# Optimization experiments

Hardware: AMD Instinct MI355X
Metric: run time of the kernel (lower is better)

Reference implementation:

```python
import jax, jax.numpy as jnp
import numpy as np

B, N, C, H = 1, 2048, 1024, 16


def setup_inputs() -> dict:
    key = jax.random.key(0)
    ks = jax.random.split(key, 8)
    scale = 1.0 / np.sqrt(C)
    d = {"x": jax.random.normal(ks[0], (B, N, C), dtype=jnp.float32)}
    for i, name in enumerate(["q1", "q2", "k1", "k2", "v", "out"]):
        d[f"W_{name}"] = jax.random.normal(ks[1 + i], (C, C), dtype=jnp.float32) * scale
        d[f"b_{name}"] = jnp.zeros((C,), dtype=jnp.float32)
    d["ln_g"] = jnp.ones((C,), dtype=jnp.float32)
    d["ln_b"] = jnp.zeros((C,), dtype=jnp.float32)
    return d


def reference(x, W_q1, b_q1, W_q2, b_q2, W_k1, b_k1, W_k2, b_k2,
              W_v, b_v, W_out, b_out, ln_g, ln_b):
    Bx, Nx, Cx = x.shape
    hd = Cx // H  # head_dim

    def proj(W, b):
        # ResidualMLP with num_layers=-1 and in_dim==out_dim: x + Linear(x)
        return x + x @ W + b

    def split_heads(z):
        return z.reshape(Bx, Nx, H, hd).transpose(0, 2, 1, 3)  # b h n d

    # kernel='identity', norm_q=norm_k=False -> raw projections
    q1 = split_heads(proj(W_q1, b_q1))
    q2 = split_heads(proj(W_q2, b_q2))
    k1 = split_heads(proj(W_k1, b_k1))
    k2 = split_heads(proj(W_k2, b_k2))
    v = split_heads(proj(W_v, b_v))

    # triple attention: elementwise product of the two Gram matrices, then
    # row-normalized (flash-style softmax; kernel also returns lse which the
    # module discards: `_, out = self.attn(...)`)
    s = jnp.einsum('bhnd,bhmd->bhnm', q1, k1) * jnp.einsum('bhnd,bhmd->bhnm', q2, k2)
    p = jax.nn.softmax(s, axis=-1)
    o = jnp.einsum('bhnm,bhmd->bhnd', p, v)

    o = o.transpose(0, 2, 1, 3).reshape(Bx, Nx, Cx)  # b n (h d)

    # LayerNorm (eps=1e-5, torch default)
    mu = o.mean(axis=-1, keepdims=True)
    var = ((o - mu) ** 2).mean(axis=-1, keepdims=True)
    o = (o - mu) / jnp.sqrt(var + 1e-5) * ln_g + ln_b

    return o @ W_out + b_out
```

## Files before the change

### kernel.cpp

```cpp
#include <hip/hip_runtime.h>
#include <hip/hip_bf16.h>
#include <stdint.h>


#define N_SEQ 2048
#define CDIM  1024
#define NHEAD 16
#define HDIM  64

typedef __attribute__((ext_vector_type(8))) short bfrag;
typedef __attribute__((ext_vector_type(4))) float f4;
typedef __attribute__((ext_vector_type(16))) float f16v;
typedef unsigned short u16;

#define MFMA16(a, b, c) __builtin_amdgcn_mfma_f32_16x16x32_bf16((a), (b), (c), 0, 0, 0)
#define MFMA32(a, b, c) __builtin_amdgcn_mfma_f32_32x32x16_bf16((a), (b), (c), 0, 0, 0)

__device__ __forceinline__ float bf2f(u16 u) {
  union { unsigned int i; float f; } c; c.i = ((unsigned int)u) << 16; return c.f;
}
__device__ __forceinline__ u16 f2bf(float f) {
  union { float f; unsigned int i; } c; c.f = f;
  unsigned int i = c.i;
  return (u16)((i + 0x7FFFu + ((i >> 16) & 1u)) >> 16);
}
__device__ __forceinline__ unsigned int pk2(float lo, float hi) {
  __hip_bfloat162 b = __float22bfloat162_rn(make_float2(lo, hi));
  unsigned int u;
  __builtin_memcpy(&u, &b, 4);
  return u;
}

__device__ __forceinline__ void gld16(const void* g, void* lds) {
  __builtin_amdgcn_global_load_lds(
      (const __attribute__((address_space(1))) void*)g,
      (__attribute__((address_space(3))) void*)lds, 16, 0, 0);
}

__global__ __launch_bounds__(256) void k_split_x(
    const float* __restrict__ x, u16* __restrict__ xh, u16* __restrict__ xl) {
  int i = (blockIdx.x * 256 + threadIdx.x) * 4;
  float4 v = *(const float4*)(x + i);
  float vv[4] = {v.x, v.y, v.z, v.w};
  ushort4 h, l;
  u16 hh[4], ll[4];
#pragma unroll
  for (int j = 0; j < 4; j++) {
    hh[j] = f2bf(vv[j]);
    ll[j] = f2bf(vv[j] - bf2f(hh[j]));
  }
  h.x = hh[0]; h.y = hh[1]; h.z = hh[2]; h.w = hh[3];
  l.x = ll[0]; l.y = ll[1]; l.z = ll[2]; l.w = ll[3];
  *(ushort4*)(xh + i) = h;
  *(ushort4*)(xl + i) = l;
}

__global__ __launch_bounds__(256) void k_wsplit(
    const float* __restrict__ W0, const float* __restrict__ W1,
    const float* __restrict__ W2, const float* __restrict__ W3,
    const float* __restrict__ W4, const float* __restrict__ W5,
    u16* __restrict__ wth, u16* __restrict__ wtl) {
  __shared__ float tile[64][65];
  int wz = blockIdx.z;
  const float* W = wz == 0 ? W0 : wz == 1 ? W1 : wz == 2 ? W2 : wz == 3 ? W3 : wz == 4 ? W4 : W5;
  int kb = blockIdx.x * 64, nb = blockIdx.y * 64;
  int t = threadIdx.x;
  int r0 = t >> 4, c0 = (t & 15) * 4;
#pragma unroll
  for (int i = 0; i < 4; i++) {
    int r = r0 + i * 16;
    float4 v = *(const float4*)(W + (size_t)(kb + r) * CDIM + nb + c0);
    tile[r][c0 + 0] = v.x; tile[r][c0 + 1] = v.y; tile[r][c0 + 2] = v.z; tile[r][c0 + 3] = v.w;
  }
  __syncthreads();
#pragma unroll
  for (int i = 0; i < 4; i++) {
    int wn = (t >> 4) + i * 16;
    int wk = (t & 15) * 4;
    ushort4 h, l;
    u16 hh[4], ll[4];
#pragma unroll
    for (int j = 0; j < 4; j++) {
      float v = tile[wk + j][wn];
      hh[j] = f2bf(v);
      ll[j] = f2bf(v - bf2f(hh[j]));
    }
    h.x = hh[0]; h.y = hh[1]; h.z = hh[2]; h.w = hh[3];
    l.x = ll[0]; l.y = ll[1]; l.z = ll[2]; l.w = ll[3];
    size_t off = ((size_t)wz * CDIM + nb + wn) * CDIM + kb + wk;
    *(ushort4*)(wth + off) = h;
    if (wz < 4) *(ushort4*)(wtl + off) = l;
  }
}

__global__ __launch_bounds__(256, 2) void k_proj(
    const u16* __restrict__ xh, const u16* __restrict__ xl,
    const u16* __restrict__ wth, const u16* __restrict__ wtl,
    const float* __restrict__ x,
    const float* __restrict__ b0, const float* __restrict__ b1,
    const float* __restrict__ b2, const float* __restrict__ b3,
    const float* __restrict__ b4,
    u16* __restrict__ qh, u16* __restrict__ ql, u16* __restrict__ vT) {
  __shared__ u16 sA[128 * 64];
  __shared__ u16 sB[128 * 64];
  int t = threadIdx.x;
  int w = blockIdx.x >> 3;
  int n0 = (blockIdx.x & 7) * 128;
  int m0 = blockIdx.y * 128;
  int lane = t & 63, wid = t >> 6;
  int wm = (wid >> 1) * 64, wn = (wid & 1) * 64;
  int lr = lane & 15, lg = lane >> 4;

  f4 acc[4][4];
#pragma unroll
  for (int i = 0; i < 4; i++)
#pragma unroll
    for (int j = 0; j < 4; j++) acc[i][j] = (f4)0.0f;

  const int nphase = (w < 4) ? 3 : 1;
  const u16* wb = wth + (size_t)w * CDIM * CDIM;
  const u16* wl = wtl + (size_t)w * CDIM * CDIM;

  int srow = t >> 3;
  int scol = (t & 7) * 8;
  int soff = srow * 64 + scol;

  for (int p = 0; p < nphase; p++) {
    const u16* A = (p == 2) ? xl : xh;
    const u16* B = (p == 1) ? wl : wb;
    for (int kt = 0; kt < CDIM; kt += 64) {
#pragma unroll
      for (int c = 0; c < 4; c++) {
        gld16(A + (size_t)(m0 + srow + c * 32) * CDIM + kt + scol, (u16*)sA + soff + c * 2048);
        gld16(B + (size_t)(n0 + srow + c * 32) * CDIM + kt + scol, (u16*)sB + soff + c * 2048);
      }
      __syncthreads();
#pragma unroll
      for (int kk = 0; kk < 2; kk++) {
        bfrag af[4], bv[4];
#pragma unroll
        for (int mi = 0; mi < 4; mi++)
          af[mi] = *(const bfrag*)(sA + (wm + mi * 16 + lr) * 64 + kk * 32 + lg * 8);
#pragma unroll
        for (int ni = 0; ni < 4; ni++)
          bv[ni] = *(const bfrag*)(sB + (wn + ni * 16 + lr) * 64 + kk * 32 + lg * 8);
#pragma unroll
        for (int mi = 0; mi < 4; mi++)
#pragma unroll
          for (int ni = 0; ni < 4; ni++)
            acc[mi][ni] = MFMA16(af[mi], bv[ni], acc[mi][ni]);
      }
      __syncthreads();
    }
  }

  const float* bias = w == 0 ? b0 : w == 1 ? b1 : w == 2 ? b2 : w == 3 ? b3 : b4;
#pragma unroll
  for (int mi = 0; mi < 4; mi++) {
#pragma unroll
    for (int ni = 0; ni < 4; ni++) {
      int col = n0 + wn + ni * 16 + lr;
      int rowb = m0 + wm + mi * 16 + lg * 4;
      float vv[4];
#pragma unroll
      for (int r = 0; r < 4; r++)
        vv[r] = acc[mi][ni][r] + x[(size_t)(rowb + r) * CDIM + col] + bias[col];
      if (w < 4) {
#pragma unroll
        for (int r = 0; r < 4; r++) {
          u16 h = f2bf(vv[r]);
          u16 l = f2bf(vv[r] - bf2f(h));
          qh[((size_t)w * N_SEQ + rowb + r) * CDIM + col] = h;
          ql[((size_t)w * N_SEQ + rowb + r) * CDIM + col] = l;
        }
      } else {
        ushort4 pv;
        pv.x = f2bf(vv[0]); pv.y = f2bf(vv[1]); pv.z = f2bf(vv[2]); pv.w = f2bf(vv[3]);
        *(ushort4*)(vT + (size_t)col * N_SEQ + rowb) = pv;
      }
    }
  }
}

__global__ __launch_bounds__(256, 2) void k_attn(
    const u16* __restrict__ qkh, const u16* __restrict__ qkl,
    const u16* __restrict__ vT, u16* __restrict__ O0, u16* __restrict__ O1,
    float2* __restrict__ ml) {
  __shared__ u16 sbuf[2][32 * 512];
  int bid = blockIdx.x;
  int khalf = bid >> 8;
  int inner = bid & 255;
  int vb = (inner & 7) * 32 + (inner >> 3);
  int h = vb >> 4;
  int qb = (vb & 15) * 128;
  int t = threadIdx.x, lane = t & 63, wv = t >> 6;
  int l31 = lane & 31, hi5 = lane >> 5;
  const size_t NC = (size_t)N_SEQ * CDIM;
  const int hoff = h * HDIM;
  const int k0 = khalf * (N_SEQ / 2);
  u16* Op = khalf ? O1 : O0;

  int qrow = qb + wv * 32 + l31;
  bfrag q1h[4], q1l[4], q2h[4], q2l[4];
#pragma unroll
  for (int ks = 0; ks < 4; ks++) {
    size_t off = (size_t)qrow * CDIM + hoff + ks * 16 + hi5 * 8;
    q1h[ks] = *(const bfrag*)(qkh + off);
    q1l[ks] = *(const bfrag*)(qkl + off);
    q2h[ks] = *(const bfrag*)(qkh + NC + off);
    q2l[ks] = *(const bfrag*)(qkl + NC + off);
  }

  const u16* kb = ((wv & 1) ? qkl : qkh) + (size_t)(2 + (wv >> 1)) * NC;

  float mrun = -1e30f, lrun = 0.f;
  f16v accO0 = (f16v)0.0f, accO1 = (f16v)0.0f;

#define STAGE(bi, kt)                                                          \
  {                                                                            \
    _Pragma("unroll") for (int i = 0; i < 8; i++) {                            \
      int kh_ = i >> 2, ksp_ = i & 3;                                          \
      gld16(kb + (size_t)((kt) + kh_ * 32 + l31) * CDIM + hoff + ksp_ * 16 +   \
                hi5 * 8,                                                       \
            sbuf[bi] + ((wv * 8 + i) << 9));                                   \
    }                                                                          \
  }

  STAGE(0, k0);
  asm volatile("s_waitcnt vmcnt(0)" ::: "memory");
  __builtin_amdgcn_s_barrier();

#pragma unroll 1
  for (int it = 0; it < N_SEQ / 2 / 64; it++) {
    int kt = k0 + it * 64;
    if (it + 1 < N_SEQ / 2 / 64) STAGE((it + 1) & 1, kt + 64);

    bfrag vld[2][4];
#pragma unroll
    for (int kh = 0; kh < 2; kh++) {
      const u16* vb0 = vT + (size_t)(hoff + l31) * N_SEQ + kt + kh * 32 + hi5 * 8;
      const u16* vb1 = vT + (size_t)(hoff + 32 + l31) * N_SEQ + kt + kh * 32 + hi5 * 8;
      vld[kh][0] = *(const bfrag*)(vb0);
      vld[kh][1] = *(const bfrag*)(vb0 + 16);
      vld[kh][2] = *(const bfrag*)(vb1);
      vld[kh][3] = *(const bfrag*)(vb1 + 16);
    }

    const u16* sb = sbuf[it & 1];
    f16v s1[2], s2[2];
#pragma unroll
    for (int kh = 0; kh < 2; kh++) { s1[kh] = (f16v)0.0f; s2[kh] = (f16v)0.0f; }
#pragma unroll
    for (int kh = 0; kh < 2; kh++) {
#pragma unroll
      for (int ks = 0; ks < 4; ks++) {
        const u16* cb = sb + ((kh * 4 + ks) << 9) + lane * 8;
        bfrag k1h = *(const bfrag*)(cb);
        bfrag k1l = *(const bfrag*)(cb + (8 << 9));
        bfrag k2h = *(const bfrag*)(cb + (16 << 9));
        bfrag k2l = *(const bfrag*)(cb + (24 << 9));
        s1[kh] = MFMA32(k1h, q1h[ks], s1[kh]);
        s1[kh] = MFMA32(k1h, q1l[ks], s1[kh]);
        s1[kh] = MFMA32(k1l, q1h[ks], s1[kh]);
        s2[kh] = MFMA32(k2h, q2h[ks], s2[kh]);
        s2[kh] = MFMA32(k2h, q2l[ks], s2[kh]);
        s2[kh] = MFMA32(k2l, q2h[ks], s2[kh]);
      }
    }
    f16v p0 = s1[0] * s2[0];
    f16v p1 = s1[1] * s2[1];

    float pm = fmaxf(p0[0], p1[0]);
#pragma unroll
    for (int j = 1; j < 16; j++) pm = fmaxf(pm, fmaxf(p0[j], p1[j]));
    pm = fmaxf(pm, __shfl_xor(pm, 32, 64));
    if (__any(pm > mrun + 8.0f)) {
      float mnew = fmaxf(mrun, pm);
      float sc = __expf(mrun - mnew);
      lrun *= sc;
#pragma unroll
      for (int j = 0; j < 16; j++) { accO0[j] *= sc; accO1[j] *= sc; }
      mrun = mnew;
    }
    float rs = 0.f;
#pragma unroll
    for (int j = 0; j < 16; j++) { p0[j] = __expf(p0[j] - mrun); rs += p0[j]; }
#pragma unroll
    for (int j = 0; j < 16; j++) { p1[j] = __expf(p1[j] - mrun); rs += p1[j]; }
    rs += __shfl_xor(rs, 32, 64);
    lrun += rs;

    unsigned dw[16];
#pragma unroll
    for (int j = 0; j < 8; j++) dw[j] = pk2(p0[2 * j], p0[2 * j + 1]);
#pragma unroll
    for (int j = 0; j < 8; j++) dw[8 + j] = pk2(p1[2 * j], p1[2 * j + 1]);

#pragma unroll
    for (int kh = 0; kh < 2; kh++) {
      unsigned j0 = dw[kh * 8 + 0], j1 = dw[kh * 8 + 1], j2 = dw[kh * 8 + 2],
               j3 = dw[kh * 8 + 3], j4 = dw[kh * 8 + 4], j5 = dw[kh * 8 + 5],
               j6 = dw[kh * 8 + 6], j7 = dw[kh * 8 + 7];
      unsigned pj0 = __shfl_xor(j0, 32, 64), pj1 = __shfl_xor(j1, 32, 64);
      unsigned pj2 = __shfl_xor(j2, 32, 64), pj3 = __shfl_xor(j3, 32, 64);
      unsigned pj4 = __shfl_xor(j4, 32, 64), pj5 = __shfl_xor(j5, 32, 64);
      unsigned pj6 = __shfl_xor(j6, 32, 64), pj7 = __shfl_xor(j7, 32, 64);
      union { unsigned u[4]; bfrag b; } f0, f1;
      f0.u[0] = hi5 ? pj2 : j0;
      f0.u[1] = hi5 ? pj3 : j1;
      f0.u[2] = hi5 ? j2 : pj0;
      f0.u[3] = hi5 ? j3 : pj1;
      f1.u[0] = hi5 ? pj6 : j4;
      f1.u[1] = hi5 ? pj7 : j5;
      f1.u[2] = hi5 ? j6 : pj4;
      f1.u[3] = hi5 ? j7 : pj5;
      accO0 = MFMA32(vld[kh][0], f0.b, accO0);
      accO0 = MFMA32(vld[kh][1], f1.b, accO0);
      accO1 = MFMA32(vld[kh][2], f0.b, accO1);
      accO1 = MFMA32(vld[kh][3], f1.b, accO1);
    }

    asm volatile("s_waitcnt vmcnt(0)" ::: "memory");
    __builtin_amdgcn_s_barrier();
  }
#undef STAGE

#pragma unroll
  for (int q4 = 0; q4 < 4; q4++) {
    ushort4 s0, s1v;
    s0.x = f2bf(accO0[q4 * 4 + 0]); s0.y = f2bf(accO0[q4 * 4 + 1]);
    s0.z = f2bf(accO0[q4 * 4 + 2]); s0.w = f2bf(accO0[q4 * 4 + 3]);
    s1v.x = f2bf(accO1[q4 * 4 + 0]); s1v.y = f2bf(accO1[q4 * 4 + 1]);
    s1v.z = f2bf(accO1[q4 * 4 + 2]); s1v.w = f2bf(accO1[q4 * 4 + 3]);
    *(ushort4*)(Op + (size_t)qrow * CDIM + hoff + q4 * 8 + hi5 * 4) = s0;
    *(ushort4*)(Op + (size_t)qrow * CDIM + hoff + 32 + q4 * 8 + hi5 * 4) = s1v;
  }
  if (!hi5) ml[(size_t)(khalf * NHEAD + h) * N_SEQ + qrow] = make_float2(mrun, lrun);
}

__global__ __launch_bounds__(256) void k_cln(
    const u16* __restrict__ O0, const u16* __restrict__ O1,
    const float2* __restrict__ ml, const float* __restrict__ g,
    const float* __restrict__ b, u16* __restrict__ oln) {
  __shared__ float rsm[4], rs2m[4];
  int row = blockIdx.x, t = threadIdx.x;
  int h = t >> 4;
  float2 a = ml[(size_t)h * N_SEQ + row];
  float2 bb = ml[(size_t)(NHEAD + h) * N_SEQ + row];
  float M = fmaxf(a.x, bb.x);
  float w0 = __expf(a.x - M), w1 = __expf(bb.x - M);
  float invL = 1.0f / (w0 * a.y + w1 * bb.y);
  ushort4 u0 = *(const ushort4*)(O0 + (size_t)row * CDIM + t * 4);
  ushort4 u1 = *(const ushort4*)(O1 + (size_t)row * CDIM + t * 4);
  float vals[4];
  vals[0] = (w0 * bf2f(u0.x) + w1 * bf2f(u1.x)) * invL;
  vals[1] = (w0 * bf2f(u0.y) + w1 * bf2f(u1.y)) * invL;
  vals[2] = (w0 * bf2f(u0.z) + w1 * bf2f(u1.z)) * invL;
  vals[3] = (w0 * bf2f(u0.w) + w1 * bf2f(u1.w)) * invL;
  float s = vals[0] + vals[1] + vals[2] + vals[3];
  float s2 = vals[0] * vals[0] + vals[1] * vals[1] + vals[2] * vals[2] + vals[3] * vals[3];
#pragma unroll
  for (int d = 1; d < 64; d <<= 1) {
    s += __shfl_xor(s, d, 64);
    s2 += __shfl_xor(s2, d, 64);
  }
  int wv = t >> 6;
  if ((t & 63) == 0) { rsm[wv] = s; rs2m[wv] = s2; }
  __syncthreads();
  s = rsm[0] + rsm[1] + rsm[2] + rsm[3];
  s2 = rs2m[0] + rs2m[1] + rs2m[2] + rs2m[3];
  float mu = s * (1.0f / CDIM);
  float var = s2 * (1.0f / CDIM) - mu * mu;
  float inv = rsqrtf(var + 1e-5f);
  ushort4 r4;
  u16 rr[4];
#pragma unroll
  for (int j = 0; j < 4; j++) {
    int col = t * 4 + j;
    rr[j] = f2bf((vals[j] - mu) * inv * g[col] + b[col]);
  }
  r4.x = rr[0]; r4.y = rr[1]; r4.z = rr[2]; r4.w = rr[3];
  *(ushort4*)(oln + (size_t)row * CDIM + t * 4) = r4;
}

__global__ __launch_bounds__(256, 2) void k_ogemm(
    const u16* __restrict__ A, const u16* __restrict__ Bw,
    const float* __restrict__ bias, float* __restrict__ out) {
  __shared__ u16 sA[128 * 64];
  __shared__ u16 sB[128 * 64];
  int t = threadIdx.x;
  int n0 = blockIdx.x * 128, m0 = blockIdx.y * 128;
  int lane = t & 63, wid = t >> 6;
  int wm = (wid >> 1) * 64, wn = (wid & 1) * 64;
  int lr = lane & 15, lg = lane >> 4;
  f4 acc[4][4];
#pragma unroll
  for (int i = 0; i < 4; i++)
#pragma unroll
    for (int j = 0; j < 4; j++) acc[i][j] = (f4)0.0f;
  int srow = t >> 3, scol = (t & 7) * 8, soff = srow * 64 + scol;
  for (int kt = 0; kt < CDIM; kt += 64) {
#pragma unroll
    for (int c = 0; c < 4; c++) {
      gld16(A + (size_t)(m0 + srow + c * 32) * CDIM + kt + scol, (u16*)sA + soff + c * 2048);
      gld16(Bw + (size_t)(n0 + srow + c * 32) * CDIM + kt + scol, (u16*)sB + soff + c * 2048);
    }
    __syncthreads();
#pragma unroll
    for (int kk = 0; kk < 2; kk++) {
      bfrag af[4], bv[4];
#pragma unroll
      for (int mi = 0; mi < 4; mi++)
        af[mi] = *(const bfrag*)(sA + (wm + mi * 16 + lr) * 64 + kk * 32 + lg * 8);
#pragma unroll
      for (int ni = 0; ni < 4; ni++)
        bv[ni] = *(const bfrag*)(sB + (wn + ni * 16 + lr) * 64 + kk * 32 + lg * 8);
#pragma unroll
      for (int mi = 0; mi < 4; mi++)
#pragma unroll
        for (int ni = 0; ni < 4; ni++)
          acc[mi][ni] = MFMA16(af[mi], bv[ni], acc[mi][ni]);
    }
    __syncthreads();
  }
#pragma unroll
  for (int mi = 0; mi < 4; mi++) {
#pragma unroll
    for (int ni = 0; ni < 4; ni++) {
      int col = n0 + wn + ni * 16 + lr;
      int rowb = m0 + wm + mi * 16 + lg * 4;
#pragma unroll
      for (int r = 0; r < 4; r++)
        out[(size_t)(rowb + r) * CDIM + col] = acc[mi][ni][r] + bias[col];
    }
  }
}

extern "C" void kernel_launch(void* const* d_in, const int* in_sizes, int n_in,
                              void* d_out, int out_size, void* d_ws, size_t ws_size,
                              hipStream_t stream) {
  const float* x   = (const float*)d_in[0];
  const float* Wq1 = (const float*)d_in[1];  const float* bq1 = (const float*)d_in[2];
  const float* Wq2 = (const float*)d_in[3];  const float* bq2 = (const float*)d_in[4];
  const float* Wk1 = (const float*)d_in[5];  const float* bk1 = (const float*)d_in[6];
  const float* Wk2 = (const float*)d_in[7];  const float* bk2 = (const float*)d_in[8];
  const float* Wv  = (const float*)d_in[9];  const float* bv  = (const float*)d_in[10];
  const float* Wo  = (const float*)d_in[11]; const float* bo  = (const float*)d_in[12];
  const float* lng = (const float*)d_in[13]; const float* lnb = (const float*)d_in[14];

  char* w = (char*)d_ws;
  u16* xh  = (u16*)(w + (0ull << 20));
  u16* xl  = (u16*)(w + (4ull << 20));
  u16* wth = (u16*)(w + (8ull << 20));
  u16* wtl = (u16*)(w + (20ull << 20));
  u16* qsh = (u16*)(w + (28ull << 20));
  u16* qsl = (u16*)(w + (44ull << 20));
  u16* vT  = (u16*)(w + (60ull << 20));
  u16* O0  = (u16*)(w + (0ull << 20));
  u16* O1  = (u16*)(w + (4ull << 20));
  float2* ml = (float2*)(w + (20ull << 20));
  u16* oln = (u16*)(w + (24ull << 20));

  k_split_x<<<2048, 256, 0, stream>>>(x, xh, xl);
  k_wsplit<<<dim3(16, 16, 6), 256, 0, stream>>>(Wq1, Wq2, Wk1, Wk2, Wv, Wo, wth, wtl);
  k_proj<<<dim3(40, 16), 256, 0, stream>>>(xh, xl, wth, wtl, x,
                                           bq1, bq2, bk1, bk2, bv, qsh, qsl, vT);
  k_attn<<<512, 256, 0, stream>>>(qsh, qsl, vT, O0, O1, ml);
  k_cln<<<2048, 256, 0, stream>>>(O0, O1, ml, lng, lnb, oln);
  k_ogemm<<<dim3(8, 16), 256, 0, stream>>>(oln, wth + 5ull * CDIM * CDIM, bo, (float*)d_out);
}
```

Baseline: 208.4 us.

## Fuse split-bf16 projection phases into one K loop with swizzled LDS

The projection kernel ran three separate passes over K (hi*hi, hi*lo, lo*hi) for the Q/K weights. Each pass reloaded the A and B tiles. Now the hi and lo tiles of both operands are loaded together in a single K loop, and all three MFMA products are issued from shared fragments, so the duplicated hi-tile global loads and loop overhead go away. An XOR swizzle on the LDS column index is added to cut bank conflicts on fragment reads. LDS use doubles to 64KB per block, which may cap occupancy near the launch bound of 2 blocks.

Measured after the change: 193.3 us. -7.3%, faster.

```diff
diff --git a/kernel.cpp b/kernel.cpp
--- a/kernel.cpp
+++ b/kernel.cpp
@@ -101,8 +101,10 @@
     const float* __restrict__ b2, const float* __restrict__ b3,
     const float* __restrict__ b4,
     u16* __restrict__ qh, u16* __restrict__ ql, u16* __restrict__ vT) {
-  __shared__ u16 sA[128 * 64];
-  __shared__ u16 sB[128 * 64];
+  __shared__ u16 sAh[128 * 64];
+  __shared__ u16 sAl[128 * 64];
+  __shared__ u16 sBh[128 * 64];
+  __shared__ u16 sBl[128 * 64];
   int t = threadIdx.x;
   int w = blockIdx.x >> 3;
   int n0 = (blockIdx.x & 7) * 128;
@@ -110,6 +112,7 @@
   int lane = t & 63, wid = t >> 6;
   int wm = (wid >> 1) * 64, wn = (wid & 1) * 64;
   int lr = lane & 15, lg = lane >> 4;
+  const bool split = (w < 4);
 
   f4 acc[4][4];
 #pragma unroll
@@ -117,41 +120,57 @@
 #pragma unroll
     for (int j = 0; j < 4; j++) acc[i][j] = (f4)0.0f;
 
-  const int nphase = (w < 4) ? 3 : 1;
-  const u16* wb = wth + (size_t)w * CDIM * CDIM;
-  const u16* wl = wtl + (size_t)w * CDIM * CDIM;
+  const u16* wbh = wth + (size_t)w * CDIM * CDIM;
+  const u16* wbl = wtl + (size_t)w * CDIM * CDIM;
 
   int srow = t >> 3;
-  int scol = (t & 7) * 8;
-  int soff = srow * 64 + scol;
-
-  for (int p = 0; p < nphase; p++) {
-    const u16* A = (p == 2) ? xl : xh;
-    const u16* B = (p == 1) ? wl : wb;
-    for (int kt = 0; kt < CDIM; kt += 64) {
-#pragma unroll
-      for (int c = 0; c < 4; c++) {
-        gld16(A + (size_t)(m0 + srow + c * 32) * CDIM + kt + scol, (u16*)sA + soff + c * 2048);
-        gld16(B + (size_t)(n0 + srow + c * 32) * CDIM + kt + scol, (u16*)sB + soff + c * 2048);
+  int scolsw = (((t & 7) ^ ((t >> 3) & 7)) * 8);
+  int soff = srow * 64 + (t & 7) * 8;
+
+  for (int kt = 0; kt < CDIM; kt += 64) {
+#pragma unroll
+    for (int c = 0; c < 4; c++) {
+      gld16(xh + (size_t)(m0 + srow + c * 32) * CDIM + kt + scolsw, sAh + soff + c * 2048);
+      gld16(wbh + (size_t)(n0 + srow + c * 32) * CDIM + kt + scolsw, sBh + soff + c * 2048);
+      if (split) {
+        gld16(xl + (size_t)(m0 + srow + c * 32) * CDIM + kt + scolsw, sAl + soff + c * 2048);
+        gld16(wbl + (size_t)(n0 + srow + c * 32) * CDIM + kt + scolsw, sBl + soff + c * 2048);
       }
-      __syncthreads();
-#pragma unroll
-      for (int kk = 0; kk < 2; kk++) {
-        bfrag af[4], bv[4];
+    }
+    __syncthreads();
+#pragma unroll
+    for (int kk = 0; kk < 2; kk++) {
+      int cc = (((kk * 4 + lg) ^ (lr & 7))) * 8;
+      bfrag afh[4], bvh[4];
+#pragma unroll
+      for (int mi = 0; mi < 4; mi++)
+        afh[mi] = *(const bfrag*)(sAh + (wm + mi * 16 + lr) * 64 + cc);
+#pragma unroll
+      for (int ni = 0; ni < 4; ni++)
+        bvh[ni] = *(const bfrag*)(sBh + (wn + ni * 16 + lr) * 64 + cc);
+#pragma unroll
+      for (int mi = 0; mi < 4; mi++)
+#pragma unroll
+        for (int ni = 0; ni < 4; ni++)
+          acc[mi][ni] = MFMA16(afh[mi], bvh[ni], acc[mi][ni]);
+      if (split) {
+        bfrag afl[4], bvl[4];
 #pragma unroll
         for (int mi = 0; mi < 4; mi++)
-          af[mi] = *(const bfrag*)(sA + (wm + mi * 16 + lr) * 64 + kk * 32 + lg * 8);
+          afl[mi] = *(const bfrag*)(sAl + (wm + mi * 16 + lr) * 64 + cc);
 #pragma unroll
         for (int ni = 0; ni < 4; ni++)
-          bv[ni] = *(const bfrag*)(sB + (wn + ni * 16 + lr) * 64 + kk * 32 + lg * 8);
+          bvl[ni] = *(const bfrag*)(sBl + (wn + ni * 16 + lr) * 64 + cc);
 #pragma unroll
         for (int mi = 0; mi < 4; mi++)
 #pragma unroll
-          for (int ni = 0; ni < 4; ni++)
-            acc[mi][ni] = MFMA16(af[mi], bv[ni], acc[mi][ni]);
+          for (int ni = 0; ni < 4; ni++) {
+            acc[mi][ni] = MFMA16(afh[mi], bvl[ni], acc[mi][ni]);
+            acc[mi][ni] = MFMA16(afl[mi], bvh[ni], acc[mi][ni]);
+          }
       }
-      __syncthreads();
-    }
+    }
+    __syncthreads();
   }
 
   const float* bias = w == 0 ? b0 : w == 1 ? b1 : w == 2 ? b2 : w == 3 ? b3 : b4;
@@ -165,7 +184,7 @@
 #pragma unroll
       for (int r = 0; r < 4; r++)
         vv[r] = acc[mi][ni][r] + x[(size_t)(rowb + r) * CDIM + col] + bias[col];
-      if (w < 4) {
+      if (split) {
 #pragma unroll
         for (int r = 0; r < 4; r++) {
           u16 h = f2bf(vv[r]);
```
